# Kernel tuning notes

Measured on AMD Instinct MI355X. Metric: run time of the kernel, lower is better.

## Reference

```python
import jax, jax.numpy as jnp
import numpy as np

N_EMB = 1024
HEAD_SIZE = 128

def setup_inputs() -> dict:
    key = jax.random.key(0)
    kx, kq, kk, kv = jax.random.split(key, 4)
    s = 1.0 / np.sqrt(N_EMB)
    return {
        "x": jax.random.normal(kx, (4, 4096, N_EMB), dtype=jnp.float32),
        "Wq": jax.random.normal(kq, (N_EMB, HEAD_SIZE), dtype=jnp.float32) * s,
        "Wk": jax.random.normal(kk, (N_EMB, HEAD_SIZE), dtype=jnp.float32) * s,
        "Wv": jax.random.normal(kv, (N_EMB, HEAD_SIZE), dtype=jnp.float32) * s,
    }

def reference(x, Wq, Wk, Wv) -> jnp.ndarray:
    B, T, C = x.shape
    q = jnp.einsum('btc,cd->btd', x, Wq)  # [B,T,H]
    k = jnp.einsum('btc,cd->btd', x, Wk)
    v = jnp.einsum('btc,cd->btd', x, Wv)
    # NOTE: original scales by sqrt(n_emb), not sqrt(head_size)
    wei = jnp.einsum('btd,bsd->bts', q, k) / jnp.sqrt(jnp.asarray(C, x.dtype))
    causal = jnp.tril(jnp.ones((T, T), dtype=bool))
    wei = jnp.where(causal, wei, -jnp.inf)
    wei = jax.nn.softmax(wei, axis=-1)
    return jnp.einsum('bts,bsd->btd', wei, v)
```

## Files before the change

### kernel.cpp

```cpp
#include <hip/hip_runtime.h>
#include <hip/hip_bf16.h>


#define TSEQ 4096
#define NBATCH 4
#define CEMB 1024
#define HS 128
#define NWORK 272

typedef float  f32x4  __attribute__((ext_vector_type(4)));
typedef float  f32x16 __attribute__((ext_vector_type(16)));
typedef __bf16 bf16x4 __attribute__((ext_vector_type(4)));
typedef __bf16 bf16x8 __attribute__((ext_vector_type(8)));
typedef int    i32x2  __attribute__((ext_vector_type(2)));
typedef int    i32x4  __attribute__((ext_vector_type(4)));

__device__ __forceinline__ __bf16 f2b(float f) { return (__bf16)f; }
__device__ __forceinline__ float fexp2(float f) { return __builtin_amdgcn_exp2f(f); }

typedef const __attribute__((address_space(1))) void* gas_ptr;
typedef __attribute__((address_space(3))) void* las_ptr;
__device__ __forceinline__ void gload16(const void* g, void* l) {
  __builtin_amdgcn_global_load_lds((gas_ptr)g, (las_ptr)l, 16, 0, 0);
}

__global__ void wtrans_kernel(const float* __restrict__ Wq,
                              const float* __restrict__ Wk,
                              const float* __restrict__ Wv,
                              __bf16* __restrict__ Wt) {
  const float* W = (blockIdx.y == 0) ? Wq : (blockIdx.y == 1) ? Wk : Wv;
  int g  = blockIdx.x * 256 + threadIdx.x;
  int n  = g & 127;
  int k0 = (g >> 7) * 8;
  bf16x8 v;
#pragma unroll
  for (int i = 0; i < 8; ++i) v[i] = f2b(W[(size_t)(k0 + i) * HS + n]);
  *(bf16x8*)(Wt + (size_t)blockIdx.y * HS * CEMB + (size_t)n * CEMB + k0) = v;
}

__global__ __launch_bounds__(128)
void proj_kernel(const float* __restrict__ x, const __bf16* __restrict__ Wt,
                 __bf16* __restrict__ qb, __bf16* __restrict__ kb,
                 __bf16* __restrict__ vt) {
  __shared__ __align__(16) __bf16 As[64 * 72];
  __shared__ __align__(16) __bf16 Bs[128 * 72];

  const int tid  = threadIdx.x;
  const int lane = tid & 63;
  const int w    = tid >> 6;
  const int l31  = lane & 31;
  const int half = lane >> 5;

  const int bid   = blockIdx.x;
  const int xcd   = bid & 7;
  const int rest  = bid >> 3;
  const int mat   = rest % 3;
  const int mslab = rest / 3;
  const int m0    = (xcd + 8 * mslab) * 64;
  const __bf16* Wm = Wt + (size_t)mat * HS * CEMB;

  f32x16 acc[2][2];
#pragma unroll
  for (int a = 0; a < 2; ++a)
#pragma unroll
    for (int b = 0; b < 2; ++b)
#pragma unroll
      for (int r = 0; r < 16; ++r) acc[a][b][r] = 0.f;

  const int srow = tid >> 3;
  const int soff = tid & 7;

  f32x4  pa[4][2];
  bf16x8 pb[8];
#pragma unroll
  for (int i = 0; i < 4; ++i) {
    const float* p = x + (size_t)(m0 + srow + 16 * i) * CEMB + soff * 8;
    pa[i][0] = *(const f32x4*)p;
    pa[i][1] = *(const f32x4*)(p + 4);
  }
#pragma unroll
  for (int i = 0; i < 8; ++i)
    pb[i] = *(const bf16x8*)(Wm + (size_t)(srow + 16 * i) * CEMB + soff * 8);

  for (int ks = 0; ks < CEMB; ks += 64) {
    __syncthreads();
#pragma unroll
    for (int i = 0; i < 4; ++i) {
      bf16x8 h;
#pragma unroll
      for (int j = 0; j < 4; ++j) {
        h[j]     = f2b(pa[i][0][j]);
        h[4 + j] = f2b(pa[i][1][j]);
      }
      *(bf16x8*)(As + (srow + 16 * i) * 72 + soff * 8) = h;
    }
#pragma unroll
    for (int i = 0; i < 8; ++i)
      *(bf16x8*)(Bs + (srow + 16 * i) * 72 + soff * 8) = pb[i];
    __syncthreads();
    if (ks + 64 < CEMB) {
#pragma unroll
      for (int i = 0; i < 4; ++i) {
        const float* p = x + (size_t)(m0 + srow + 16 * i) * CEMB + ks + 64 + soff * 8;
        pa[i][0] = *(const f32x4*)p;
        pa[i][1] = *(const f32x4*)(p + 4);
      }
#pragma unroll
      for (int i = 0; i < 8; ++i)
        pb[i] = *(const bf16x8*)(Wm + (size_t)(srow + 16 * i) * CEMB + ks + 64 + soff * 8);
    }
#pragma unroll
    for (int kc = 0; kc < 4; ++kc) {
      bf16x8 af[2], bf[2];
#pragma unroll
      for (int mi = 0; mi < 2; ++mi)
        af[mi] = *(const bf16x8*)(As + (mi * 32 + l31) * 72 + kc * 16 + half * 8);
#pragma unroll
      for (int ni = 0; ni < 2; ++ni)
        bf[ni] = *(const bf16x8*)(Bs + (64 * w + ni * 32 + l31) * 72 + kc * 16 + half * 8);
#pragma unroll
      for (int mi = 0; mi < 2; ++mi)
#pragma unroll
        for (int ni = 0; ni < 2; ++ni)
          acc[mi][ni] = __builtin_amdgcn_mfma_f32_32x32x16_bf16(
              af[mi], bf[ni], acc[mi][ni], 0, 0, 0);
    }
  }

  const float qscale = 1.4426950408889634f / 32.0f;
  if (mat == 0) {
#pragma unroll
    for (int mi = 0; mi < 2; ++mi)
#pragma unroll
      for (int ni = 0; ni < 2; ++ni) {
        int n = 64 * w + ni * 32 + l31;
#pragma unroll
        for (int r = 0; r < 16; ++r) {
          int m = m0 + mi * 32 + (r & 3) + 8 * (r >> 2) + 4 * half;
          qb[(size_t)m * HS + n] = f2b(acc[mi][ni][r] * qscale);
        }
      }
  } else if (mat == 1) {
#pragma unroll
    for (int mi = 0; mi < 2; ++mi)
#pragma unroll
      for (int ni = 0; ni < 2; ++ni) {
        int n = 64 * w + ni * 32 + l31;
#pragma unroll
        for (int r = 0; r < 16; ++r) {
          int m = m0 + mi * 32 + (r & 3) + 8 * (r >> 2) + 4 * half;
          kb[(size_t)m * HS + n] = f2b(acc[mi][ni][r]);
        }
      }
  } else {
    const int bt = m0 >> 12;
#pragma unroll
    for (int mi = 0; mi < 2; ++mi)
#pragma unroll
      for (int ni = 0; ni < 2; ++ni) {
        int n = 64 * w + ni * 32 + l31;
#pragma unroll
        for (int g = 0; g < 4; ++g) {
          bf16x4 pk;
#pragma unroll
          for (int d = 0; d < 4; ++d) pk[d] = f2b(acc[mi][ni][4 * g + d]);
          int tl = ((m0 + mi * 32) & 4095) + 8 * g + 4 * half;
          *(bf16x4*)(vt + ((size_t)bt * HS + n) * TSEQ + tl) = pk;
        }
      }
  }
}

__global__ __launch_bounds__(256)
void attn_kernel(const __bf16* __restrict__ qb, const __bf16* __restrict__ kb,
                 const __bf16* __restrict__ vt,
                 __bf16* __restrict__ Opart, float* __restrict__ Lpart) {
  __shared__ __align__(16) __bf16 Kt[2][64 * 128];
  __shared__ __align__(16) __bf16 Vt[2][128 * 64];

  const int tid   = threadIdx.x;
  const int lane  = tid & 63;
  const int w     = tid >> 6;
  const int l31   = lane & 31;
  const int half  = lane >> 5;
  const int batch = blockIdx.y;
  const int xw    = blockIdx.x;

  int q = 0;
  while (q < 31 && xw >= (((q + 2) * (q + 2)) >> 2)) ++q;
  const int split = xw - (((q + 1) * (q + 1)) >> 2);
  const int ntile = 2 * (q + 1);
  const int nsp   = (q + 2) >> 1;
  const int tps   = (ntile + nsp - 1) / nsp;
  const int it0   = split * tps;
  const int it1   = min(it0 + tps, ntile);

  const int strip0 = q * 128 + w * 32;
  const size_t bbase = (size_t)batch * TSEQ;

  bf16x8 qf[8];
  {
    const __bf16* qr = qb + (bbase + strip0 + l31) * HS + half * 8;
#pragma unroll
    for (int kc = 0; kc < 8; ++kc) qf[kc] = *(const bf16x8*)(qr + kc * 16);
  }

  const __bf16* kbb = kb + bbase * HS;
  const __bf16* vbb = vt + (size_t)batch * HS * TSEQ;

  auto stage = [&](int buf, int c0) {
#pragma unroll
    for (int i = 0; i < 4; ++i) {
      int idx  = w * 256 + i * 64 + lane;
      int krow = idx >> 4;
      int kug  = (idx & 15) ^ (krow & 7);
      gload16(kbb + (size_t)(c0 + krow) * HS + kug * 8,
              &Kt[buf][(w * 256 + i * 64) * 8]);
      int d   = idx >> 3;
      int vug = (idx & 7) ^ (d & 7);
      gload16(vbb + (size_t)d * TSEQ + c0 + vug * 8,
              &Vt[buf][(w * 256 + i * 64) * 8]);
    }
  };

  f32x16 o[4];
#pragma unroll
  for (int nt = 0; nt < 4; ++nt)
#pragma unroll
    for (int r = 0; r < 16; ++r) o[nt][r] = 0.f;
  float lsum = 0.f;

  int cur = 0;
  stage(0, it0 * 64);

  for (int it = it0; it < it1; ++it) {
    const int c0 = it * 64;
    asm volatile("s_waitcnt vmcnt(0)" ::: "memory");
    __syncthreads();
    if (it + 1 < it1) stage(cur ^ 1, c0 + 64);

    if (c0 <= strip0 + 31) {
      i32x2 pkt[2][4];
#pragma unroll
      for (int t = 0; t < 2; ++t)
#pragma unroll
        for (int j = 0; j < 4; ++j) pkt[t][j] = (i32x2){0, 0};

#pragma unroll
      for (int t = 0; t < 2; ++t) {
        if (c0 + t * 32 <= strip0 + 31) {
          f32x16 s;
#pragma unroll
          for (int r = 0; r < 16; ++r) s[r] = 0.f;
          __builtin_amdgcn_s_setprio(1);
#pragma unroll
          for (int kc = 0; kc < 8; ++kc) {
            int u = 2 * kc + half;
            bf16x8 kf = *(const bf16x8*)(
                &Kt[cur][(t * 32 + l31) * 128 + ((u ^ (l31 & 7)) * 8)]);
            s = __builtin_amdgcn_mfma_f32_32x32x16_bf16(kf, qf[kc], s, 0, 0, 0);
          }
          __builtin_amdgcn_s_setprio(0);
          if (c0 + t * 32 + 31 > strip0) {
#pragma unroll
            for (int r = 0; r < 16; ++r) {
              int key = c0 + t * 32 + (r & 3) + 8 * (r >> 2) + 4 * half;
              if (key > strip0 + l31) s[r] = -INFINITY;
            }
          }
          float p[16], ps = 0.f;
#pragma unroll
          for (int r = 0; r < 16; ++r) { p[r] = fexp2(s[r]); ps += p[r]; }
          lsum += ps;
#pragma unroll
          for (int j = 0; j < 4; ++j) {
            bf16x4 t4;
#pragma unroll
            for (int d = 0; d < 4; ++d) t4[d] = f2b(p[4 * j + d]);
            pkt[t][j] = __builtin_bit_cast(i32x2, t4);
          }
        }
      }
#pragma unroll
      for (int kk = 0; kk < 4; ++kk) {
        int t = kk >> 1, lo = (kk & 1) * 2;
        i32x2 a = pkt[t][lo], b = pkt[t][lo + 1];
        i32x4 af4;
#if defined(__has_builtin) && __has_builtin(__builtin_amdgcn_permlane32_swap)
        {
          auto r0 = __builtin_amdgcn_permlane32_swap(a.x, b.x, false, false);
          auto r1 = __builtin_amdgcn_permlane32_swap(a.y, b.y, false, false);
          af4.x = r0[0]; af4.y = r1[0]; af4.z = r0[1]; af4.w = r1[1];
        }
#else
        {
          i32x2 ra, rb;
          ra.x = __shfl_xor(a.x, 32); ra.y = __shfl_xor(a.y, 32);
          rb.x = __shfl_xor(b.x, 32); rb.y = __shfl_xor(b.y, 32);
          af4.x = half ? rb.x : a.x;
          af4.y = half ? rb.y : a.y;
          af4.z = half ? b.x  : ra.x;
          af4.w = half ? b.y  : ra.y;
        }
#endif
        bf16x8 af = __builtin_bit_cast(bf16x8, af4);
        __builtin_amdgcn_s_setprio(1);
#pragma unroll
        for (int nt = 0; nt < 4; ++nt) {
          int u = 2 * kk + half;
          bf16x8 vf = *(const bf16x8*)(
              &Vt[cur][(nt * 32 + l31) * 64 + ((u ^ (l31 & 7)) * 8)]);
          o[nt] = __builtin_amdgcn_mfma_f32_32x32x16_bf16(af, vf, o[nt], 0, 0, 0);
        }
        __builtin_amdgcn_s_setprio(0);
      }
    }
    cur ^= 1;
  }

  const size_t widx = (size_t)batch * NWORK + xw;
  __bf16* Op = Opart + widx * (128 * 128);
#pragma unroll
  for (int r = 0; r < 16; ++r) {
    int rloc = w * 32 + 4 * half + (r & 3) + 8 * (r >> 2);
#pragma unroll
    for (int nt = 0; nt < 4; ++nt)
      Op[rloc * 128 + nt * 32 + l31] = f2b(o[nt][r]);
  }
  lsum += __shfl_xor(lsum, 32);
  if (half == 0) Lpart[widx * 128 + w * 32 + l31] = lsum;
}

__global__ __launch_bounds__(256)
void reduce_kernel(const __bf16* __restrict__ Opart, const float* __restrict__ Lpart,
                   float* __restrict__ out) {
  const int batch = blockIdx.y;
  const int rowg  = blockIdx.x * 8 + (threadIdx.x >> 5);
  const int q = rowg >> 7;
  const int nsp = (q + 2) >> 1;
  const int off = ((q + 1) * (q + 1)) >> 2;
  const size_t wbase = (size_t)batch * NWORK + off;
  const int row128 = rowg & 127;
  const int c0 = (threadIdx.x & 31) * 4;

  float l = 0.f;
  for (int s = 0; s < nsp; ++s) l += Lpart[(wbase + s) * 128 + row128];
  const float inv = 1.0f / l;

  const __bf16* op = Opart + wbase * (128 * 128) + row128 * 128 + c0;
  f32x4 a = {0.f, 0.f, 0.f, 0.f};
  for (int s = 0; s < nsp; ++s) {
    bf16x4 v = *(const bf16x4*)(op + (size_t)s * 128 * 128);
#pragma unroll
    for (int j = 0; j < 4; ++j) a[j] += (float)v[j];
  }
  a *= inv;
  *(f32x4*)(out + ((size_t)batch * TSEQ + rowg) * HS + c0) = a;
}

extern "C" void kernel_launch(void* const* d_in, const int* in_sizes, int n_in,
                              void* d_out, int out_size, void* d_ws, size_t ws_size,
                              hipStream_t stream) {
  const float* x  = (const float*)d_in[0];
  const float* Wq = (const float*)d_in[1];
  const float* Wk = (const float*)d_in[2];
  const float* Wv = (const float*)d_in[3];
  float* out = (float*)d_out;

  char* ws = (char*)d_ws;
  __bf16* Wt = (__bf16*)ws;
  __bf16* qb = (__bf16*)(ws + 786432);
  __bf16* kb = (__bf16*)(ws + 786432 + 4194304);
  __bf16* vt = (__bf16*)(ws + 786432 + 2 * 4194304);
  __bf16* Opart = (__bf16*)(ws + 786432 + 3 * 4194304);
  float*  Lpart = (float*)(ws + 786432 + 3 * 4194304 +
                           (size_t)NBATCH * NWORK * 128 * 128 * 2);

  wtrans_kernel<<<dim3(64, 3), 256, 0, stream>>>(Wq, Wk, Wv, Wt);
  proj_kernel<<<dim3(768), 128, 0, stream>>>(x, Wt, qb, kb, vt);
  attn_kernel<<<dim3(NWORK, NBATCH), 256, 0, stream>>>(qb, kb, vt, Opart, Lpart);
  reduce_kernel<<<dim3(512, NBATCH), 256, 0, stream>>>(Opart, Lpart, out);
}
```

Baseline: 168.6 us.

## Use 512-thread attention blocks covering 256-row query strips with fixed 4-tile splits

The attention kernel now runs 8 waves per block, each covering 32 query rows, so every block handles a 256-row strip. Each work item processes exactly four 64-key tiles, which halves the number of work items and reshapes the split-K partitioning. The reduce kernel and workspace layout are updated to match. Each staged K/V tile is now shared by twice as many query rows, cutting global and LDS traffic per row, at the cost of fewer blocks and possibly lower occupancy from the larger block.

```diff
diff --git a/kernel.cpp b/kernel.cpp
--- a/kernel.cpp
+++ b/kernel.cpp
@@ -6,7 +6,7 @@
 #define NBATCH 4
 #define CEMB 1024
 #define HS 128
-#define NWORK 272
+#define NWORK 136
 
 typedef float  f32x4  __attribute__((ext_vector_type(4)));
 typedef float  f32x16 __attribute__((ext_vector_type(16)));
@@ -171,7 +171,7 @@
   }
 }
 
-__global__ __launch_bounds__(256)
+__global__ __launch_bounds__(512)
 void attn_kernel(const __bf16* __restrict__ qb, const __bf16* __restrict__ kb,
                  const __bf16* __restrict__ vt,
                  __bf16* __restrict__ Opart, float* __restrict__ Lpart) {
@@ -186,16 +186,13 @@
   const int batch = blockIdx.y;
   const int xw    = blockIdx.x;
 
-  int q = 0;
-  while (q < 31 && xw >= (((q + 2) * (q + 2)) >> 2)) ++q;
-  const int split = xw - (((q + 1) * (q + 1)) >> 2);
-  const int ntile = 2 * (q + 1);
-  const int nsp   = (q + 2) >> 1;
-  const int tps   = (ntile + nsp - 1) / nsp;
-  const int it0   = split * tps;
-  const int it1   = min(it0 + tps, ntile);
-
-  const int strip0 = q * 128 + w * 32;
+  int q0 = 0;
+  while (q0 < 15 && xw >= (((q0 + 1) * (q0 + 2)) >> 1)) ++q0;
+  const int split = xw - ((q0 * (q0 + 1)) >> 1);
+  const int it0   = split * 4;
+  const int it1   = it0 + 4;
+
+  const int strip0 = q0 * 256 + w * 32;
   const size_t bbase = (size_t)batch * TSEQ;
 
   bf16x8 qf[8];
@@ -210,16 +207,16 @@
 
   auto stage = [&](int buf, int c0) {
 #pragma unroll
-    for (int i = 0; i < 4; ++i) {
-      int idx  = w * 256 + i * 64 + lane;
+    for (int i = 0; i < 2; ++i) {
+      int idx  = i * 512 + w * 64 + lane;
       int krow = idx >> 4;
       int kug  = (idx & 15) ^ (krow & 7);
       gload16(kbb + (size_t)(c0 + krow) * HS + kug * 8,
-              &Kt[buf][(w * 256 + i * 64) * 8]);
+              &Kt[buf][(i * 512 + w * 64) * 8]);
       int d   = idx >> 3;
       int vug = (idx & 7) ^ (d & 7);
       gload16(vbb + (size_t)d * TSEQ + c0 + vug * 8,
-              &Vt[buf][(w * 256 + i * 64) * 8]);
+              &Vt[buf][(i * 512 + w * 64) * 8]);
     }
   };
 
@@ -319,7 +316,7 @@
   }
 
   const size_t widx = (size_t)batch * NWORK + xw;
-  __bf16* Op = Opart + widx * (128 * 128);
+  __bf16* Op = Opart + widx * (256 * 128);
 #pragma unroll
   for (int r = 0; r < 16; ++r) {
     int rloc = w * 32 + 4 * half + (r & 3) + 8 * (r >> 2);
@@ -328,7 +325,7 @@
       Op[rloc * 128 + nt * 32 + l31] = f2b(o[nt][r]);
   }
   lsum += __shfl_xor(lsum, 32);
-  if (half == 0) Lpart[widx * 128 + w * 32 + l31] = lsum;
+  if (half == 0) Lpart[widx * 256 + w * 32 + l31] = lsum;
 }
 
 __global__ __launch_bounds__(256)
@@ -336,21 +333,21 @@
                    float* __restrict__ out) {
   const int batch = blockIdx.y;
   const int rowg  = blockIdx.x * 8 + (threadIdx.x >> 5);
-  const int q = rowg >> 7;
-  const int nsp = (q + 2) >> 1;
-  const int off = ((q + 1) * (q + 1)) >> 2;
+  const int q0 = rowg >> 8;
+  const int nsp = q0 + 1;
+  const int off = (q0 * (q0 + 1)) >> 1;
   const size_t wbase = (size_t)batch * NWORK + off;
-  const int row128 = rowg & 127;
+  const int row256 = rowg & 255;
   const int c0 = (threadIdx.x & 31) * 4;
 
   float l = 0.f;
-  for (int s = 0; s < nsp; ++s) l += Lpart[(wbase + s) * 128 + row128];
+  for (int s = 0; s < nsp; ++s) l += Lpart[(wbase + s) * 256 + row256];
   const float inv = 1.0f / l;
 
-  const __bf16* op = Opart + wbase * (128 * 128) + row128 * 128 + c0;
+  const __bf16* op = Opart + wbase * (256 * 128) + row256 * 128 + c0;
   f32x4 a = {0.f, 0.f, 0.f, 0.f};
   for (int s = 0; s < nsp; ++s) {
-    bf16x4 v = *(const bf16x4*)(op + (size_t)s * 128 * 128);
+    bf16x4 v = *(const bf16x4*)(op + (size_t)s * 256 * 128);
 #pragma unroll
     for (int j = 0; j < 4; ++j) a[j] += (float)v[j];
   }
@@ -374,10 +371,10 @@
   __bf16* vt = (__bf16*)(ws + 786432 + 2 * 4194304);
   __bf16* Opart = (__bf16*)(ws + 786432 + 3 * 4194304);
   float*  Lpart = (float*)(ws + 786432 + 3 * 4194304 +
-                           (size_t)NBATCH * NWORK * 128 * 128 * 2);
+                           (size_t)NBATCH * NWORK * 256 * 128 * 2);
 
   wtrans_kernel<<<dim3(64, 3), 256, 0, stream>>>(Wq, Wk, Wv, Wt);
   proj_kernel<<<dim3(768), 128, 0, stream>>>(x, Wt, qb, kb, vt);
-  attn_kernel<<<dim3(NWORK, NBATCH), 256, 0, stream>>>(qb, kb, vt, Opart, Lpart);
+  attn_kernel<<<dim3(NWORK, NBATCH), 512, 0, stream>>>(qb, kb, vt, Opart, Lpart);
   reduce_kernel<<<dim3(512, NBATCH), 256, 0, stream>>>(Opart, Lpart, out);
 }
```

Result: no change. 168.9 us (+0.2%).
